# Kernel optimization log

Hardware: AMD Instinct MI355X
Metric: run time of the kernel (lower is better)

The kernel has to match this reference:

```python
import jax, jax.numpy as jnp
import numpy as np
from jax import lax

B, T, I, H = 4096, 64, 8, 128


def _lstm_layer(xs, W_ih, W_hh, b):
    # xs: [T, B, D_in]; PyTorch gate order i, f, g, o
    def step(carry, x_t):
        h, c = carry
        gates = x_t @ W_ih.T + h @ W_hh.T + b  # [B, 4H]
        i, f, g, o = jnp.split(gates, 4, axis=-1)
        i = jax.nn.sigmoid(i)
        f = jax.nn.sigmoid(f)
        g = jnp.tanh(g)
        o = jax.nn.sigmoid(o)
        c_new = f * c + i * g
        h_new = o * jnp.tanh(c_new)
        return (h_new, c_new), h_new

    n_b = xs.shape[1]
    h0 = jnp.zeros((n_b, W_hh.shape[1]), xs.dtype)
    c0 = jnp.zeros((n_b, W_hh.shape[1]), xs.dtype)
    (h_last, _), ys = lax.scan(step, (h0, c0), xs)
    return ys, h_last


def setup_inputs() -> dict:
    key = jax.random.key(0)
    ks = jax.random.split(key, 14)
    s = 1.0 / np.sqrt(H)
    u = lambda k, shape: jax.random.uniform(k, shape, jnp.float32, -s, s)
    return {
        "x": jax.random.normal(ks[0], (B, T, I), jnp.float32),
        "W_ih0": u(ks[1], (4 * H, I)),
        "W_hh0": u(ks[2], (4 * H, H)),
        "b_ih0": u(ks[3], (4 * H,)),
        "b_hh0": u(ks[4], (4 * H,)),
        "W_ih1": u(ks[5], (4 * H, H)),
        "W_hh1": u(ks[6], (4 * H, H)),
        "b_ih1": u(ks[7], (4 * H,)),
        "b_hh1": u(ks[8], (4 * H,)),
        "W_d1": u(ks[9], (5, H)),
        "b_d1": u(ks[10], (5,)),
        "W_d2": u(ks[11], (1, 5)),
        "b_d2": u(ks[12], (1,)),
    }


def reference(x, W_ih0, W_hh0, b_ih0, b_hh0, W_ih1, W_hh1, b_ih1, b_hh1,
              W_d1, b_d1, W_d2, b_d2):
    xs = jnp.transpose(x, (1, 0, 2))  # [T, B, I]
    ys0, _ = _lstm_layer(xs, W_ih0, W_hh0, b_ih0 + b_hh0)
    # inter-layer dropout (p=0.2) and trailing Dropout are identity in eval mode
    _, h_last = _lstm_layer(ys0, W_ih1, W_hh1, b_ih1 + b_hh1)  # [B, H]
    out = jax.nn.relu(h_last)
    out = jax.nn.relu(out @ W_d1.T + b_d1)  # [B, 5]
    out = out @ W_d2.T + b_d2  # [B, 1]
    return out
```

## Files before the change

kernel.cpp:

```cpp
#include <hip/hip_runtime.h>

typedef _Float16 h8 __attribute__((ext_vector_type(8)));
typedef _Float16 h4 __attribute__((ext_vector_type(4)));
typedef float f4 __attribute__((ext_vector_type(4)));

#define B_ 4096
#define T_ 64
#define I_ 8
#define H_ 128

#define WC0_OFF 0
#define H0_OFF  131072
#define H1_OFF  139264
#define LDS_TOTAL 147456

#define LOG2E    1.4426950408889634f
#define TWOLOG2E 2.8853900817779268f

__device__ __forceinline__ float sigm2_(float v) {
    return __builtin_amdgcn_rcpf(1.f + exp2f(-v));
}
__device__ __forceinline__ float tanh2_(float v) {
    return 1.f - 2.f * __builtin_amdgcn_rcpf(exp2f(v) + 1.f);
}
__device__ __forceinline__ float tanhn_(float v) {
    return 1.f - 2.f * __builtin_amdgcn_rcpf(exp2f(TWOLOG2E * v) + 1.f);
}

__global__ __launch_bounds__(512, 2) void lstm_fused_kernel(
    const float* __restrict__ x,
    const float* __restrict__ Wih0, const float* __restrict__ Whh0,
    const float* __restrict__ bih0, const float* __restrict__ bhh0,
    const float* __restrict__ Wih1, const float* __restrict__ Whh1,
    const float* __restrict__ bih1, const float* __restrict__ bhh1,
    const float* __restrict__ Wd1, const float* __restrict__ bd1,
    const float* __restrict__ Wd2, const float* __restrict__ bd2,
    float* __restrict__ out)
{
    __shared__ __align__(16) unsigned char lds[LDS_TOTAL];
    const int tid = threadIdx.x;
    const int w   = tid >> 6;
    const int l   = tid & 63;
    const int c16 = l & 15;
    const int G4  = l >> 4;
    const int rowbase = blockIdx.x * 16;
    const int swzl = (l & 7) << 4;

    {
        const int p  = tid;
        const int q  = p & 3;
        const int gs = q * H_ + (p >> 6) * 16 + ((p >> 2) & 3) * 4 + ((p >> 4) & 3);
        const float sc = (q == 2) ? TWOLOG2E : LOG2E;
        const float* src = Whh0 + (size_t)gs * H_;
        const int swz = (p & 7) << 4;
        unsigned char* dst = lds + WC0_OFF + p * 256;
#pragma unroll
        for (int kb = 0; kb < 16; kb++) {
            float4 f0 = *(const float4*)(src + kb * 8);
            float4 f1 = *(const float4*)(src + kb * 8 + 4);
            h8 v;
            v[0]=(_Float16)(f0.x*sc); v[1]=(_Float16)(f0.y*sc);
            v[2]=(_Float16)(f0.z*sc); v[3]=(_Float16)(f0.w*sc);
            v[4]=(_Float16)(f1.x*sc); v[5]=(_Float16)(f1.y*sc);
            v[6]=(_Float16)(f1.z*sc); v[7]=(_Float16)(f1.w*sc);
            *(h8*)(dst + ((kb * 16) ^ swz)) = v;
        }
    }
    {
        f4 z = {0.f, 0.f, 0.f, 0.f};
        if (tid < 256) *(f4*)(lds + H0_OFF + 4096 + tid * 16) = z;
        else           *(f4*)(lds + H1_OFF + 4096 + (tid - 256) * 16) = z;
    }

    h8 wc1[4][8];
    h4 ax16[4];
    f4 b1[4];
    {
        const int rq = c16 & 3;
        const float sc1 = (rq == 2) ? TWOLOG2E : LOG2E;
#pragma unroll
        for (int j = 0; j < 4; j++) {
            const int gs = rq * H_ + w * 16 + (c16 >> 2) * 4 + j;
#pragma unroll
            for (int ks = 0; ks < 8; ks++) {
                const int k0 = ks * 32 + G4 * 8;
                const float* src = (k0 < 128) ? (Whh1 + (size_t)gs * H_ + k0)
                                              : (Wih1 + (size_t)gs * H_ + (k0 - 128));
                float4 f0 = *(const float4*)src;
                float4 f1 = *(const float4*)(src + 4);
                h8 v;
                v[0]=(_Float16)(f0.x*sc1); v[1]=(_Float16)(f0.y*sc1);
                v[2]=(_Float16)(f0.z*sc1); v[3]=(_Float16)(f0.w*sc1);
                v[4]=(_Float16)(f1.x*sc1); v[5]=(_Float16)(f1.y*sc1);
                v[6]=(_Float16)(f1.z*sc1); v[7]=(_Float16)(f1.w*sc1);
                wc1[j][ks] = v;
            }
            h4 a;
#pragma unroll
            for (int e = 0; e < 4; e++) {
                const int k = G4 * 4 + e;
                float val = 0.f;
                if (k < 8)       val = Wih0[(size_t)gs * I_ + k] * sc1;
                else if (k == 8) val = (bih0[gs] + bhh0[gs]) * sc1;
                a[e] = (_Float16)val;
            }
            ax16[j] = a;
            f4 bb;
#pragma unroll
            for (int q2 = 0; q2 < 4; q2++) {
                const int gs2 = q2 * H_ + w * 16 + G4 * 4 + j;
                bb[q2] = (bih1[gs2] + bhh1[gs2]) * ((q2 == 2) ? TWOLOG2E : LOG2E);
            }
            b1[j] = bb;
        }
    }

    const float* xrow = x + (size_t)(rowbase + c16) * T_ * I_;
    float4 xf0 = *(const float4*)(xrow);
    float4 xf1 = *(const float4*)(xrow + 4);

    float c0r[4] = {0.f, 0.f, 0.f, 0.f};
    float c1r[4] = {0.f, 0.f, 0.f, 0.f};

    __syncthreads();

    int cur = 0;
    for (int t = 0; t < T_; t++) {
        h4 bx;
        bx[0] = (_Float16)0.f; bx[1] = (_Float16)0.f;
        bx[2] = (_Float16)0.f; bx[3] = (_Float16)0.f;
        if (G4 == 0) {
            bx[0]=(_Float16)xf0.x; bx[1]=(_Float16)xf0.y;
            bx[2]=(_Float16)xf0.z; bx[3]=(_Float16)xf0.w;
        } else if (G4 == 1) {
            bx[0]=(_Float16)xf1.x; bx[1]=(_Float16)xf1.y;
            bx[2]=(_Float16)xf1.z; bx[3]=(_Float16)xf1.w;
        } else if (G4 == 2) {
            bx[0] = (_Float16)1.f;
        }
        if (t < T_ - 1) {
            xf0 = *(const float4*)(xrow + (t + 1) * 8);
            xf1 = *(const float4*)(xrow + (t + 1) * 8 + 4);
        }

        f4 acc[4];
        {
            f4 z = {0.f, 0.f, 0.f, 0.f};
#pragma unroll
            for (int j = 0; j < 4; j++) acc[j] = z;
        }
        const unsigned char* h0rd = lds + H0_OFF + (cur ^ 1) * 4096;
#pragma unroll
        for (int ks = 0; ks < 4; ks++) {
            h8 b = *(const h8*)(h0rd + ((c16 * 256 + ks * 64 + G4 * 16) ^ swzl));
#pragma unroll
            for (int j = 0; j < 4; j++) {
                h8 a = *(const h8*)(lds + WC0_OFF + (w * 64 + j * 16 + c16) * 256
                                    + ((ks * 64 + G4 * 16) ^ swzl));
                acc[j] = __builtin_amdgcn_mfma_f32_16x16x32_f16(a, b, acc[j], 0, 0, 0);
            }
        }
#pragma unroll
        for (int j = 0; j < 4; j++)
            acc[j] = __builtin_amdgcn_mfma_f32_16x16x16f16(ax16[j], bx, acc[j], 0, 0, 0);

        unsigned char* h0wr = lds + H0_OFF + cur * 4096;
        {
            h4 hv;
#pragma unroll
            for (int j = 0; j < 4; j++) {
                const float vi = sigm2_(acc[j][0]);
                const float vf = sigm2_(acc[j][1]);
                const float vg = tanh2_(acc[j][2]);
                const float vo = sigm2_(acc[j][3]);
                const float cn = vf * c0r[j] + vi * vg;
                c0r[j] = cn;
                hv[j] = (_Float16)(vo * tanhn_(cn));
            }
            *(h4*)(h0wr + ((c16 * 256 + w * 32 + G4 * 8) ^ swzl)) = hv;
        }

        __syncthreads();

        const unsigned char* h1rd = lds + H1_OFF + (cur ^ 1) * 4096;
        const unsigned char* h0n  = lds + H0_OFF + cur * 4096;
#pragma unroll
        for (int j = 0; j < 4; j++) acc[j] = b1[j];
#pragma unroll
        for (int ks = 0; ks < 4; ks++) {
            h8 b = *(const h8*)(h1rd + ((c16 * 256 + ks * 64 + G4 * 16) ^ swzl));
#pragma unroll
            for (int j = 0; j < 4; j++)
                acc[j] = __builtin_amdgcn_mfma_f32_16x16x32_f16(wc1[j][ks], b, acc[j], 0, 0, 0);
        }
#pragma unroll
        for (int ks = 0; ks < 4; ks++) {
            h8 b = *(const h8*)(h0n + ((c16 * 256 + ks * 64 + G4 * 16) ^ swzl));
#pragma unroll
            for (int j = 0; j < 4; j++)
                acc[j] = __builtin_amdgcn_mfma_f32_16x16x32_f16(wc1[j][ks + 4], b, acc[j], 0, 0, 0);
        }
        unsigned char* h1wr = lds + H1_OFF + cur * 4096;
        {
            h4 hv;
#pragma unroll
            for (int j = 0; j < 4; j++) {
                const float vi = sigm2_(acc[j][0]);
                const float vf = sigm2_(acc[j][1]);
                const float vg = tanh2_(acc[j][2]);
                const float vo = sigm2_(acc[j][3]);
                const float cn = vf * c1r[j] + vi * vg;
                c1r[j] = cn;
                hv[j] = (_Float16)(vo * tanhn_(cn));
            }
            *(h4*)(h1wr + ((c16 * 256 + w * 32 + G4 * 8) ^ swzl)) = hv;
        }
        cur ^= 1;
    }

    __syncthreads();

    if (tid < 128) {
        const int r = tid >> 3, part = tid & 7;
        const unsigned char* h1f = lds + H1_OFF + 4096;
        const int rswz = (r & 7) << 4;
        float s0 = 0.f, s1 = 0.f, s2 = 0.f, s3 = 0.f, s4 = 0.f;
#pragma unroll
        for (int kk = 0; kk < 16; kk++) {
            const int k = part * 16 + kk;
            float a = (float)*(const _Float16*)(h1f + ((r * 256 + k * 2) ^ rswz));
            a = fmaxf(a, 0.f);
            s0 += a * Wd1[0 * H_ + k];
            s1 += a * Wd1[1 * H_ + k];
            s2 += a * Wd1[2 * H_ + k];
            s3 += a * Wd1[3 * H_ + k];
            s4 += a * Wd1[4 * H_ + k];
        }
#pragma unroll
        for (int m = 1; m < 8; m <<= 1) {
            s0 += __shfl_xor(s0, m);
            s1 += __shfl_xor(s1, m);
            s2 += __shfl_xor(s2, m);
            s3 += __shfl_xor(s3, m);
            s4 += __shfl_xor(s4, m);
        }
        if (part == 0) {
            float o = bd2[0];
            o += fmaxf(s0 + bd1[0], 0.f) * Wd2[0];
            o += fmaxf(s1 + bd1[1], 0.f) * Wd2[1];
            o += fmaxf(s2 + bd1[2], 0.f) * Wd2[2];
            o += fmaxf(s3 + bd1[3], 0.f) * Wd2[3];
            o += fmaxf(s4 + bd1[4], 0.f) * Wd2[4];
            out[rowbase + r] = o;
        }
    }
}

extern "C" void kernel_launch(void* const* d_in, const int* in_sizes, int n_in,
                              void* d_out, int out_size, void* d_ws, size_t ws_size,
                              hipStream_t stream)
{
    const float* x    = (const float*)d_in[0];
    const float* Wih0 = (const float*)d_in[1];
    const float* Whh0 = (const float*)d_in[2];
    const float* bih0 = (const float*)d_in[3];
    const float* bhh0 = (const float*)d_in[4];
    const float* Wih1 = (const float*)d_in[5];
    const float* Whh1 = (const float*)d_in[6];
    const float* bih1 = (const float*)d_in[7];
    const float* bhh1 = (const float*)d_in[8];
    const float* Wd1  = (const float*)d_in[9];
    const float* bd1  = (const float*)d_in[10];
    const float* Wd2  = (const float*)d_in[11];
    const float* bd2  = (const float*)d_in[12];

    lstm_fused_kernel<<<B_ / 16, 512, 0, stream>>>(
        x, Wih0, Whh0, bih0, bhh0, Wih1, Whh1, bih1, bhh1,
        Wd1, bd1, Wd2, bd2, (float*)d_out);
}
```

Before: 202.0 us.

## Hoist layer-1 recurrent MFMAs before the barrier and add per-step end barrier

```diff
diff --git a/kernel.cpp b/kernel.cpp
--- a/kernel.cpp
+++ b/kernel.cpp
@@ -27,7 +27,7 @@
     return 1.f - 2.f * __builtin_amdgcn_rcpf(exp2f(TWOLOG2E * v) + 1.f);
 }
 
-__global__ __launch_bounds__(512, 2) void lstm_fused_kernel(
+__global__ __launch_bounds__(512, 1) void lstm_fused_kernel(
     const float* __restrict__ x,
     const float* __restrict__ Wih0, const float* __restrict__ Whh0,
     const float* __restrict__ bih0, const float* __restrict__ bhh0,
@@ -143,11 +143,11 @@
             xf1 = *(const float4*)(xrow + (t + 1) * 8 + 4);
         }
 
-        f4 acc[4];
+        f4 acc0[4], acc1[4];
         {
             f4 z = {0.f, 0.f, 0.f, 0.f};
 #pragma unroll
-            for (int j = 0; j < 4; j++) acc[j] = z;
+            for (int j = 0; j < 4; j++) acc0[j] = z;
         }
         const unsigned char* h0rd = lds + H0_OFF + (cur ^ 1) * 4096;
 #pragma unroll
@@ -157,22 +157,33 @@
             for (int j = 0; j < 4; j++) {
                 h8 a = *(const h8*)(lds + WC0_OFF + (w * 64 + j * 16 + c16) * 256
                                     + ((ks * 64 + G4 * 16) ^ swzl));
-                acc[j] = __builtin_amdgcn_mfma_f32_16x16x32_f16(a, b, acc[j], 0, 0, 0);
+                acc0[j] = __builtin_amdgcn_mfma_f32_16x16x32_f16(a, b, acc0[j], 0, 0, 0);
             }
         }
 #pragma unroll
         for (int j = 0; j < 4; j++)
-            acc[j] = __builtin_amdgcn_mfma_f32_16x16x16f16(ax16[j], bx, acc[j], 0, 0, 0);
+            acc0[j] = __builtin_amdgcn_mfma_f32_16x16x16f16(ax16[j], bx, acc0[j], 0, 0, 0);
+
+        const unsigned char* h1rd = lds + H1_OFF + (cur ^ 1) * 4096;
+#pragma unroll
+        for (int j = 0; j < 4; j++) acc1[j] = b1[j];
+#pragma unroll
+        for (int ks = 0; ks < 4; ks++) {
+            h8 b = *(const h8*)(h1rd + ((c16 * 256 + ks * 64 + G4 * 16) ^ swzl));
+#pragma unroll
+            for (int j = 0; j < 4; j++)
+                acc1[j] = __builtin_amdgcn_mfma_f32_16x16x32_f16(wc1[j][ks], b, acc1[j], 0, 0, 0);
+        }
 
         unsigned char* h0wr = lds + H0_OFF + cur * 4096;
         {
             h4 hv;
 #pragma unroll
             for (int j = 0; j < 4; j++) {
-                const float vi = sigm2_(acc[j][0]);
-                const float vf = sigm2_(acc[j][1]);
-                const float vg = tanh2_(acc[j][2]);
-                const float vo = sigm2_(acc[j][3]);
+                const float vi = sigm2_(acc0[j][0]);
+                const float vf = sigm2_(acc0[j][1]);
+                const float vg = tanh2_(acc0[j][2]);
+                const float vo = sigm2_(acc0[j][3]);
                 const float cn = vf * c0r[j] + vi * vg;
                 c0r[j] = cn;
                 hv[j] = (_Float16)(vo * tanhn_(cn));
@@ -182,43 +193,33 @@
 
         __syncthreads();
 
-        const unsigned char* h1rd = lds + H1_OFF + (cur ^ 1) * 4096;
-        const unsigned char* h0n  = lds + H0_OFF + cur * 4096;
-#pragma unroll
-        for (int j = 0; j < 4; j++) acc[j] = b1[j];
-#pragma unroll
-        for (int ks = 0; ks < 4; ks++) {
-            h8 b = *(const h8*)(h1rd + ((c16 * 256 + ks * 64 + G4 * 16) ^ swzl));
-#pragma unroll
-            for (int j = 0; j < 4; j++)
-                acc[j] = __builtin_amdgcn_mfma_f32_16x16x32_f16(wc1[j][ks], b, acc[j], 0, 0, 0);
-        }
+        const unsigned char* h0n = lds + H0_OFF + cur * 4096;
 #pragma unroll
         for (int ks = 0; ks < 4; ks++) {
             h8 b = *(const h8*)(h0n + ((c16 * 256 + ks * 64 + G4 * 16) ^ swzl));
 #pragma unroll
             for (int j = 0; j < 4; j++)
-                acc[j] = __builtin_amdgcn_mfma_f32_16x16x32_f16(wc1[j][ks + 4], b, acc[j], 0, 0, 0);
+                acc1[j] = __builtin_amdgcn_mfma_f32_16x16x32_f16(wc1[j][ks + 4], b, acc1[j], 0, 0, 0);
         }
         unsigned char* h1wr = lds + H1_OFF + cur * 4096;
         {
             h4 hv;
 #pragma unroll
             for (int j = 0; j < 4; j++) {
-                const float vi = sigm2_(acc[j][0]);
-                const float vf = sigm2_(acc[j][1]);
-                const float vg = tanh2_(acc[j][2]);
-                const float vo = sigm2_(acc[j][3]);
+                const float vi = sigm2_(acc1[j][0]);
+                const float vf = sigm2_(acc1[j][1]);
+                const float vg = tanh2_(acc1[j][2]);
+                const float vo = sigm2_(acc1[j][3]);
                 const float cn = vf * c1r[j] + vi * vg;
                 c1r[j] = cn;
                 hv[j] = (_Float16)(vo * tanhn_(cn));
             }
             *(h4*)(h1wr + ((c16 * 256 + w * 32 + G4 * 8) ^ swzl)) = hv;
         }
+
+        __syncthreads();
         cur ^= 1;
     }
-
-    __syncthreads();
 
     if (tid < 128) {
         const int r = tid >> 3, part = tid & 7;
```

Result: slower. 209.7 us (+3.8%).

## Split LSTM into prep kernel and layer-sequential chunked recurrence with streamed h0

Applied to the files above, without the earlier changes.

```diff
diff --git a/kernel.cpp b/kernel.cpp
--- a/kernel.cpp
+++ b/kernel.cpp
@@ -9,14 +9,25 @@
 #define I_ 8
 #define H_ 128
 
-#define WC0_OFF 0
-#define H0_OFF  131072
-#define H1_OFF  139264
-#define LDS_TOTAL 147456
-
 #define LOG2E    1.4426950408889634f
 #define TWOLOG2E 2.8853900817779268f
 
+#define WREG 0
+#define H0P  131072
+#define H1P  139264
+#define STG  147456
+#define BB   155648
+#define LDS_TOTAL 157696
+
+#define XH_WS    0
+#define WC0P_WS  4194304
+#define WC1A_WS  4325376
+#define WC1B_WS  4456448
+#define WC0R_WS  4587520
+#define AXI_WS   4653056
+#define B1I_WS   4669440
+#define STRM_WS  4671488
+
 __device__ __forceinline__ float sigm2_(float v) {
     return __builtin_amdgcn_rcpf(1.f + exp2f(-v));
 }
@@ -26,16 +37,73 @@
 __device__ __forceinline__ float tanhn_(float v) {
     return 1.f - 2.f * __builtin_amdgcn_rcpf(exp2f(TWOLOG2E * v) + 1.f);
 }
-
-__global__ __launch_bounds__(512, 2) void lstm_fused_kernel(
+__device__ __forceinline__ int gs_of(int p) {
+    return (p & 3) * H_ + (p >> 6) * 16 + ((p >> 2) & 3) * 4 + ((p >> 4) & 3);
+}
+__device__ __forceinline__ float scl_(int q) { return (q == 2) ? TWOLOG2E : LOG2E; }
+
+__global__ __launch_bounds__(256) void prep_kernel(
     const float* __restrict__ x,
     const float* __restrict__ Wih0, const float* __restrict__ Whh0,
     const float* __restrict__ bih0, const float* __restrict__ bhh0,
     const float* __restrict__ Wih1, const float* __restrict__ Whh1,
     const float* __restrict__ bih1, const float* __restrict__ bhh1,
+    _Float16* __restrict__ xh, _Float16* __restrict__ wc0p,
+    _Float16* __restrict__ wc1a, _Float16* __restrict__ wc1b,
+    _Float16* __restrict__ wc0r, _Float16* __restrict__ axI,
+    float* __restrict__ b1I)
+{
+    const int i = blockIdx.x * 256 + threadIdx.x;
+    if (i < B_ * T_ * I_) xh[i] = (_Float16)x[i];
+    if (i < 65536) {
+        const int p = i >> 7, k = i & 127;
+        const int gs = gs_of(p);
+        const float sc = scl_(p & 3);
+        const int hidx = p * 128 + (((k >> 3) * 16 ^ ((p & 7) << 4)) >> 1) + (k & 7);
+        wc0p[hidx] = (_Float16)(Whh0[gs * H_ + k] * sc);
+        wc1a[hidx] = (_Float16)(Whh1[gs * H_ + k] * sc);
+    }
+    if (i < 65536) {
+        const int tid = i >> 7, rem = i & 127;
+        const int jj = rem >> 5, ks = (rem >> 3) & 3, e = rem & 7;
+        const int w = tid >> 6, l = tid & 63, c16 = l & 15, G4 = l >> 4;
+        const int p = w * 64 + jj * 16 + c16;
+        const int gs = gs_of(p);
+        const int k = ks * 32 + G4 * 8 + e;
+        wc1b[i] = (_Float16)(Wih1[gs * H_ + k] * scl_(c16 & 3));
+    }
+    if (i < 32768) {
+        const int tid = i >> 6, rem = i & 63;
+        const int jj = rem >> 5, ks = (rem >> 3) & 3, e = rem & 7;
+        const int w = tid >> 6, l = tid & 63, c16 = l & 15, G4 = l >> 4;
+        const int p = w * 64 + jj * 16 + c16;
+        const int gs = gs_of(p);
+        const int k = ks * 32 + G4 * 8 + e;
+        wc0r[i] = (_Float16)(Whh0[gs * H_ + k] * scl_(c16 & 3));
+    }
+    if (i < 8192) {
+        const int tid = i >> 4, rem = i & 15;
+        const int jj = rem >> 2, e = rem & 3;
+        const int w = tid >> 6, l = tid & 63, c16 = l & 15, G4 = l >> 4;
+        const int p = w * 64 + jj * 16 + c16;
+        const int gs = gs_of(p);
+        const int k = G4 * 4 + e;
+        float v = 0.f;
+        if (k < 8)       v = Wih0[gs * I_ + k] * scl_(c16 & 3);
+        else if (k == 8) v = (bih0[gs] + bhh0[gs]) * scl_(c16 & 3);
+        axI[i] = (_Float16)v;
+    }
+    if (i < 512) b1I[i] = (bih1[gs_of(i)] + bhh1[gs_of(i)]) * scl_(i & 3);
+}
+
+__global__ __launch_bounds__(512) void lstm_main(
+    const _Float16* __restrict__ xh, const _Float16* __restrict__ wc0p,
+    const _Float16* __restrict__ wc1a, const _Float16* __restrict__ wc1bI,
+    const _Float16* __restrict__ wc0rI, const _Float16* __restrict__ axI,
+    const float* __restrict__ b1I, char* __restrict__ h0s,
     const float* __restrict__ Wd1, const float* __restrict__ bd1,
     const float* __restrict__ Wd2, const float* __restrict__ bd2,
-    float* __restrict__ out)
+    float* __restrict__ out, int Tc)
 {
     __shared__ __align__(16) unsigned char lds[LDS_TOTAL];
     const int tid = threadIdx.x;
@@ -43,186 +111,165 @@
     const int l   = tid & 63;
     const int c16 = l & 15;
     const int G4  = l >> 4;
-    const int rowbase = blockIdx.x * 16;
+    const int bk  = blockIdx.x;
+    const int rowbase = bk * 16;
     const int swzl = (l & 7) << 4;
 
-    {
-        const int p  = tid;
-        const int q  = p & 3;
-        const int gs = q * H_ + (p >> 6) * 16 + ((p >> 2) & 3) * 4 + ((p >> 4) & 3);
-        const float sc = (q == 2) ? TWOLOG2E : LOG2E;
-        const float* src = Whh0 + (size_t)gs * H_;
-        const int swz = (p & 7) << 4;
-        unsigned char* dst = lds + WC0_OFF + p * 256;
-#pragma unroll
-        for (int kb = 0; kb < 16; kb++) {
-            float4 f0 = *(const float4*)(src + kb * 8);
-            float4 f1 = *(const float4*)(src + kb * 8 + 4);
-            h8 v;
-            v[0]=(_Float16)(f0.x*sc); v[1]=(_Float16)(f0.y*sc);
-            v[2]=(_Float16)(f0.z*sc); v[3]=(_Float16)(f0.w*sc);
-            v[4]=(_Float16)(f1.x*sc); v[5]=(_Float16)(f1.y*sc);
-            v[6]=(_Float16)(f1.z*sc); v[7]=(_Float16)(f1.w*sc);
-            *(h8*)(dst + ((kb * 16) ^ swz)) = v;
-        }
-    }
-    {
-        f4 z = {0.f, 0.f, 0.f, 0.f};
-        if (tid < 256) *(f4*)(lds + H0_OFF + 4096 + tid * 16) = z;
-        else           *(f4*)(lds + H1_OFF + 4096 + (tid - 256) * 16) = z;
-    }
-
-    h8 wc1[4][8];
-    h4 ax16[4];
-    f4 b1[4];
-    {
-        const int rq = c16 & 3;
-        const float sc1 = (rq == 2) ? TWOLOG2E : LOG2E;
-#pragma unroll
-        for (int j = 0; j < 4; j++) {
-            const int gs = rq * H_ + w * 16 + (c16 >> 2) * 4 + j;
-#pragma unroll
-            for (int ks = 0; ks < 8; ks++) {
-                const int k0 = ks * 32 + G4 * 8;
-                const float* src = (k0 < 128) ? (Whh1 + (size_t)gs * H_ + k0)
-                                              : (Wih1 + (size_t)gs * H_ + (k0 - 128));
-                float4 f0 = *(const float4*)src;
-                float4 f1 = *(const float4*)(src + 4);
-                h8 v;
-                v[0]=(_Float16)(f0.x*sc1); v[1]=(_Float16)(f0.y*sc1);
-                v[2]=(_Float16)(f0.z*sc1); v[3]=(_Float16)(f0.w*sc1);
-                v[4]=(_Float16)(f1.x*sc1); v[5]=(_Float16)(f1.y*sc1);
-                v[6]=(_Float16)(f1.z*sc1); v[7]=(_Float16)(f1.w*sc1);
-                wc1[j][ks] = v;
-            }
-            h4 a;
-#pragma unroll
-            for (int e = 0; e < 4; e++) {
-                const int k = G4 * 4 + e;
-                float val = 0.f;
-                if (k < 8)       val = Wih0[(size_t)gs * I_ + k] * sc1;
-                else if (k == 8) val = (bih0[gs] + bhh0[gs]) * sc1;
-                a[e] = (_Float16)val;
-            }
-            ax16[j] = a;
-            f4 bb;
-#pragma unroll
-            for (int q2 = 0; q2 < 4; q2++) {
-                const int gs2 = q2 * H_ + w * 16 + G4 * 4 + j;
-                bb[q2] = (bih1[gs2] + bhh1[gs2]) * ((q2 == 2) ? TWOLOG2E : LOG2E);
-            }
-            b1[j] = bb;
-        }
-    }
-
-    const float* xrow = x + (size_t)(rowbase + c16) * T_ * I_;
-    float4 xf0 = *(const float4*)(xrow);
-    float4 xf1 = *(const float4*)(xrow + 4);
+    *(unsigned long long*)(lds + H0P + tid * 8) = 0ull;
+    *(unsigned long long*)(lds + H1P + tid * 8) = 0ull;
+    ((float*)(lds + BB))[tid] = b1I[tid];
+
+    h4 ax[4];
+#pragma unroll
+    for (int j = 0; j < 4; j++)
+        ax[j] = *(const h4*)(axI + tid * 16 + j * 4);
 
     float c0r[4] = {0.f, 0.f, 0.f, 0.f};
     float c1r[4] = {0.f, 0.f, 0.f, 0.f};
 
-    __syncthreads();
-
-    int cur = 0;
-    for (int t = 0; t < T_; t++) {
-        h4 bx;
-        bx[0] = (_Float16)0.f; bx[1] = (_Float16)0.f;
-        bx[2] = (_Float16)0.f; bx[3] = (_Float16)0.f;
-        if (G4 == 0) {
-            bx[0]=(_Float16)xf0.x; bx[1]=(_Float16)xf0.y;
-            bx[2]=(_Float16)xf0.z; bx[3]=(_Float16)xf0.w;
-        } else if (G4 == 1) {
-            bx[0]=(_Float16)xf1.x; bx[1]=(_Float16)xf1.y;
-            bx[2]=(_Float16)xf1.z; bx[3]=(_Float16)xf1.w;
-        } else if (G4 == 2) {
-            bx[0] = (_Float16)1.f;
-        }
-        if (t < T_ - 1) {
-            xf0 = *(const float4*)(xrow + (t + 1) * 8);
-            xf1 = *(const float4*)(xrow + (t + 1) * 8 + 4);
-        }
-
-        f4 acc[4];
-        {
-            f4 z = {0.f, 0.f, 0.f, 0.f};
-#pragma unroll
-            for (int j = 0; j < 4; j++) acc[j] = z;
-        }
-        const unsigned char* h0rd = lds + H0_OFF + (cur ^ 1) * 4096;
-#pragma unroll
-        for (int ks = 0; ks < 4; ks++) {
-            h8 b = *(const h8*)(h0rd + ((c16 * 256 + ks * 64 + G4 * 16) ^ swzl));
-#pragma unroll
-            for (int j = 0; j < 4; j++) {
-                h8 a = *(const h8*)(lds + WC0_OFF + (w * 64 + j * 16 + c16) * 256
-                                    + ((ks * 64 + G4 * 16) ^ swzl));
-                acc[j] = __builtin_amdgcn_mfma_f32_16x16x32_f16(a, b, acc[j], 0, 0, 0);
-            }
-        }
+    for (int t0 = 0; t0 < T_; t0 += Tc) {
+#pragma unroll
+        for (int i = 0; i < 16; i++)
+            *(f4*)(lds + WREG + tid * 256 + i * 16) =
+                *(const f4*)((const char*)wc0p + tid * 256 + i * 16);
+        h8 wc0r[2][4];
+#pragma unroll
+        for (int j = 0; j < 2; j++)
+#pragma unroll
+            for (int ks = 0; ks < 4; ks++)
+                wc0r[j][ks] = *(const h8*)(wc0rI + tid * 64 + j * 32 + ks * 8);
+        __syncthreads();
+
+        h4 xpre;
+        if (G4 < 2)
+            xpre = *(const h4*)(xh + ((size_t)(rowbase + c16) * T_ + t0) * I_ + G4 * 4);
+
+        for (int t = t0; t < t0 + Tc; t++) {
+            h4 bx;
+            bx[0] = (_Float16)0.f; bx[1] = (_Float16)0.f;
+            bx[2] = (_Float16)0.f; bx[3] = (_Float16)0.f;
+            if (G4 < 2) bx = xpre;
+            else if (G4 == 2) bx[0] = (_Float16)1.f;
+            if (t + 1 < T_ && G4 < 2)
+                xpre = *(const h4*)(xh + ((size_t)(rowbase + c16) * T_ + t + 1) * I_ + G4 * 4);
+
+            f4 acc[4];
+            {
+                f4 z = {0.f, 0.f, 0.f, 0.f};
+#pragma unroll
+                for (int j = 0; j < 4; j++) acc[j] = z;
+            }
+            const unsigned char* h0rd = lds + H0P + (t & 1) * 4096;
+#pragma unroll
+            for (int ks = 0; ks < 4; ks++) {
+                h8 b = *(const h8*)(h0rd + ((c16 * 256 + ks * 64 + G4 * 16) ^ swzl));
+#pragma unroll
+                for (int j = 0; j < 2; j++)
+                    acc[j] = __builtin_amdgcn_mfma_f32_16x16x32_f16(wc0r[j][ks], b, acc[j], 0, 0, 0);
+#pragma unroll
+                for (int j = 2; j < 4; j++) {
+                    h8 a = *(const h8*)(lds + WREG + (w * 64 + j * 16 + c16) * 256
+                                        + ((ks * 64 + G4 * 16) ^ swzl));
+                    acc[j] = __builtin_amdgcn_mfma_f32_16x16x32_f16(a, b, acc[j], 0, 0, 0);
+                }
+            }
+#pragma unroll
+            for (int j = 0; j < 4; j++)
+                acc[j] = __builtin_amdgcn_mfma_f32_16x16x16f16(ax[j], bx, acc[j], 0, 0, 0);
+
+            unsigned char* h0wr = lds + H0P + ((t + 1) & 1) * 4096;
+            {
+                h4 hv;
+#pragma unroll
+                for (int j = 0; j < 4; j++) {
+                    const float vi = sigm2_(acc[j][0]);
+                    const float vf = sigm2_(acc[j][1]);
+                    const float vg = tanh2_(acc[j][2]);
+                    const float vo = sigm2_(acc[j][3]);
+                    const float cn = vf * c0r[j] + vi * vg;
+                    c0r[j] = cn;
+                    hv[j] = (_Float16)(vo * tanhn_(cn));
+                }
+                *(h4*)(h0wr + ((c16 * 256 + w * 32 + G4 * 8) ^ swzl)) = hv;
+            }
+            __syncthreads();
+            if (tid < 256) {
+                f4 v = *(const f4*)(lds + H0P + ((t + 1) & 1) * 4096 + tid * 16);
+                *(f4*)(h0s + ((size_t)bk * Tc + (t - t0)) * 4096 + tid * 16) = v;
+            }
+        }
+
+#pragma unroll
+        for (int i = 0; i < 16; i++)
+            *(f4*)(lds + WREG + tid * 256 + i * 16) =
+                *(const f4*)((const char*)wc1a + tid * 256 + i * 16);
+        h8 wc1b[4][4];
 #pragma unroll
         for (int j = 0; j < 4; j++)
-            acc[j] = __builtin_amdgcn_mfma_f32_16x16x16f16(ax16[j], bx, acc[j], 0, 0, 0);
-
-        unsigned char* h0wr = lds + H0_OFF + cur * 4096;
-        {
-            h4 hv;
-#pragma unroll
-            for (int j = 0; j < 4; j++) {
-                const float vi = sigm2_(acc[j][0]);
-                const float vf = sigm2_(acc[j][1]);
-                const float vg = tanh2_(acc[j][2]);
-                const float vo = sigm2_(acc[j][3]);
-                const float cn = vf * c0r[j] + vi * vg;
-                c0r[j] = cn;
-                hv[j] = (_Float16)(vo * tanhn_(cn));
-            }
-            *(h4*)(h0wr + ((c16 * 256 + w * 32 + G4 * 8) ^ swzl)) = hv;
-        }
-
+#pragma unroll
+            for (int ks = 0; ks < 4; ks++)
+                wc1b[j][ks] = *(const h8*)(wc1bI + tid * 128 + j * 32 + ks * 8);
+        if (tid < 256) {
+            f4 v = *(const f4*)(h0s + ((size_t)bk * Tc) * 4096 + tid * 16);
+            *(f4*)(lds + STG + (t0 & 1) * 4096 + tid * 16) = v;
+        }
         __syncthreads();
 
-        const unsigned char* h1rd = lds + H1_OFF + (cur ^ 1) * 4096;
-        const unsigned char* h0n  = lds + H0_OFF + cur * 4096;
-#pragma unroll
-        for (int j = 0; j < 4; j++) acc[j] = b1[j];
-#pragma unroll
-        for (int ks = 0; ks < 4; ks++) {
-            h8 b = *(const h8*)(h1rd + ((c16 * 256 + ks * 64 + G4 * 16) ^ swzl));
+        for (int t = t0; t < t0 + Tc; t++) {
+            const bool pv = (t + 1 < t0 + Tc);
+            f4 pre;
+            if (pv && tid < 256)
+                pre = *(const f4*)(h0s + ((size_t)bk * Tc + (t + 1 - t0)) * 4096 + tid * 16);
+
+            f4 acc[4];
 #pragma unroll
             for (int j = 0; j < 4; j++)
-                acc[j] = __builtin_amdgcn_mfma_f32_16x16x32_f16(wc1[j][ks], b, acc[j], 0, 0, 0);
-        }
-#pragma unroll
-        for (int ks = 0; ks < 4; ks++) {
-            h8 b = *(const h8*)(h0n + ((c16 * 256 + ks * 64 + G4 * 16) ^ swzl));
-#pragma unroll
-            for (int j = 0; j < 4; j++)
-                acc[j] = __builtin_amdgcn_mfma_f32_16x16x32_f16(wc1[j][ks + 4], b, acc[j], 0, 0, 0);
-        }
-        unsigned char* h1wr = lds + H1_OFF + cur * 4096;
-        {
-            h4 hv;
-#pragma unroll
-            for (int j = 0; j < 4; j++) {
-                const float vi = sigm2_(acc[j][0]);
-                const float vf = sigm2_(acc[j][1]);
-                const float vg = tanh2_(acc[j][2]);
-                const float vo = sigm2_(acc[j][3]);
-                const float cn = vf * c1r[j] + vi * vg;
-                c1r[j] = cn;
-                hv[j] = (_Float16)(vo * tanhn_(cn));
-            }
-            *(h4*)(h1wr + ((c16 * 256 + w * 32 + G4 * 8) ^ swzl)) = hv;
-        }
-        cur ^= 1;
-    }
-
-    __syncthreads();
+                acc[j] = *(const f4*)(lds + BB + (w * 64 + j * 16 + G4 * 4) * 4);
+
+            const unsigned char* h1rd = lds + H1P + (t & 1) * 4096;
+            const unsigned char* strd = lds + STG + (t & 1) * 4096;
+#pragma unroll
+            for (int ks = 0; ks < 4; ks++) {
+                h8 b = *(const h8*)(h1rd + ((c16 * 256 + ks * 64 + G4 * 16) ^ swzl));
+#pragma unroll
+                for (int j = 0; j < 4; j++) {
+                    h8 a = *(const h8*)(lds + WREG + (w * 64 + j * 16 + c16) * 256
+                                        + ((ks * 64 + G4 * 16) ^ swzl));
+                    acc[j] = __builtin_amdgcn_mfma_f32_16x16x32_f16(a, b, acc[j], 0, 0, 0);
+                }
+            }
+#pragma unroll
+            for (int ks = 0; ks < 4; ks++) {
+                h8 b = *(const h8*)(strd + ((c16 * 256 + ks * 64 + G4 * 16) ^ swzl));
+#pragma unroll
+                for (int j = 0; j < 4; j++)
+                    acc[j] = __builtin_amdgcn_mfma_f32_16x16x32_f16(wc1b[j][ks], b, acc[j], 0, 0, 0);
+            }
+
+            unsigned char* h1wr = lds + H1P + ((t + 1) & 1) * 4096;
+            {
+                h4 hv;
+#pragma unroll
+                for (int j = 0; j < 4; j++) {
+                    const float vi = sigm2_(acc[j][0]);
+                    const float vf = sigm2_(acc[j][1]);
+                    const float vg = tanh2_(acc[j][2]);
+                    const float vo = sigm2_(acc[j][3]);
+                    const float cn = vf * c1r[j] + vi * vg;
+                    c1r[j] = cn;
+                    hv[j] = (_Float16)(vo * tanhn_(cn));
+                }
+                *(h4*)(h1wr + ((c16 * 256 + w * 32 + G4 * 8) ^ swzl)) = hv;
+            }
+            if (pv && tid < 256)
+                *(f4*)(lds + STG + ((t + 1) & 1) * 4096 + tid * 16) = pre;
+            __syncthreads();
+        }
+    }
 
     if (tid < 128) {
         const int r = tid >> 3, part = tid & 7;
-        const unsigned char* h1f = lds + H1_OFF + 4096;
+        const unsigned char* h1f = lds + H1P;
         const int rswz = (r & 7) << 4;
         float s0 = 0.f, s1 = 0.f, s2 = 0.f, s3 = 0.f, s4 = 0.f;
 #pragma unroll
@@ -274,7 +321,26 @@
     const float* Wd2  = (const float*)d_in[11];
     const float* bd2  = (const float*)d_in[12];
 
-    lstm_fused_kernel<<<B_ / 16, 512, 0, stream>>>(
+    char* ws = (char*)d_ws;
+    _Float16* xh   = (_Float16*)(ws + XH_WS);
+    _Float16* wc0p = (_Float16*)(ws + WC0P_WS);
+    _Float16* wc1a = (_Float16*)(ws + WC1A_WS);
+    _Float16* wc1b = (_Float16*)(ws + WC1B_WS);
+    _Float16* wc0r = (_Float16*)(ws + WC0R_WS);
+    _Float16* axI  = (_Float16*)(ws + AXI_WS);
+    float*    b1I  = (float*)(ws + B1I_WS);
+    char*     h0s  = ws + STRM_WS;
+
+    int Tc = 1;
+    for (int c : {64, 32, 16, 8, 4, 2}) {
+        if (STRM_WS + (size_t)256 * c * 4096 <= ws_size) { Tc = c; break; }
+    }
+
+    prep_kernel<<<8192, 256, 0, stream>>>(
         x, Wih0, Whh0, bih0, bhh0, Wih1, Whh1, bih1, bhh1,
-        Wd1, bd1, Wd2, bd2, (float*)d_out);
-}
+        xh, wc0p, wc1a, wc1b, wc0r, axI, b1I);
+
+    lstm_main<<<B_ / 16, 512, 0, stream>>>(
+        xh, wc0p, wc1a, wc1b, wc0r, axI, b1I, h0s,
+        Wd1, bd1, Wd2, bd2, (float*)d_out, Tc);
+}
```

After: 227.3 us. 12.5% more time.
